# Kernel optimization log

Measured on AMD Instinct MI355X. Metric: run time of the kernel, lower is better.

## Reference

```python
import jax, jax.numpy as jnp
import numpy as np

N_NODES = 100000
N_EDGES = 800000
IN_FEATS = 128
NUM_CLASSES = 64


def setup_inputs() -> dict:
    key = jax.random.key(0)
    k1, k2, k3, k4 = jax.random.split(key, 4)
    x = jax.random.normal(k1, (N_NODES, IN_FEATS), dtype=jnp.float32)
    edge_src = jax.random.randint(k2, (N_EDGES,), 0, N_NODES, dtype=jnp.int64)
    edge_dst = jax.random.randint(k3, (N_EDGES,), 0, N_NODES, dtype=jnp.int64)
    W_neigh = jax.random.normal(k4, (NUM_CLASSES, IN_FEATS), dtype=jnp.float32) * (1.0 / np.sqrt(IN_FEATS))
    b_neigh = jnp.zeros((NUM_CLASSES,), dtype=jnp.float32)
    return {"x": x, "edge_src": edge_src, "edge_dst": edge_dst,
            "W_neigh": W_neigh, "b_neigh": b_neigh}


def reference(x, edge_src, edge_dst, W_neigh, b_neigh):
    # DGL SAGEConv with aggregator_type='gcn':
    #   h_neigh[v] = (sum_{u->v} x[u] + x[v]) / (in_degree(v) + 1)
    #   out = h_neigh @ W_neigh^T + b_neigh
    n = x.shape[0]
    # gather source features per edge, scatter-sum into destinations
    neigh_sum = jax.ops.segment_sum(x[edge_src], edge_dst, num_segments=n)  # [N, F]
    deg = jax.ops.segment_sum(jnp.ones((edge_src.shape[0],), dtype=x.dtype),
                              edge_dst, num_segments=n)                     # [N]
    h = (neigh_sum + x) / (deg + 1.0)[:, None]
    out = jnp.einsum('nf,cf->nc', h, W_neigh) + b_neigh
    return out
```

## Files before the change

### kernel.cpp

```cpp
#include <hip/hip_runtime.h>

#define N_NODES 100000
#define N_EDGES 800000
#define IN_FEATS 128
#define NUM_CLASSES 64

#define NSB    98
#define SCAP   9216
#define BINCAP 56
#define NBKT   12500
#define NBKT_PAD (NSB * 128)
#define HCAP   88
#define BKCAP  176

#define K1_GRID 1955

typedef short bf16x8 __attribute__((ext_vector_type(8)));
typedef float f32x4  __attribute__((ext_vector_type(4)));

static __device__ __forceinline__ unsigned short f2bf(float f) {
    unsigned u = __float_as_uint(f);
    unsigned r = (u + 0x7fffu + ((u >> 16) & 1u)) >> 16;
    return (unsigned short)r;
}
static __device__ __forceinline__ float bf2f(unsigned short v) {
    return __uint_as_float(((unsigned)v) << 16);
}

static __device__ __forceinline__ void gemm_body(char* smem, int gid,
                                                 const float* __restrict__ x,
                                                 const float* __restrict__ W,
                                                 unsigned short* __restrict__ y16) {
    const long base = (long)gid * 64;
    if (base >= N_NODES) return;

    unsigned short* Wf = (unsigned short*)smem;
    typedef unsigned short XsRow[136];
    XsRow* Xs = (XsRow*)(smem + 16384);

    const int tid = threadIdx.x;

    for (int i = tid; i < 4 * 4 * 64 * 8; i += 256) {
        const int j    = i & 7;
        const int lane = (i >> 3) & 63;
        const int t    = (i >> 9) & 3;
        const int s    = i >> 11;
        const int k = s * 32 + ((lane >> 4) << 3) + j;
        const int c = t * 16 + (lane & 15);
        Wf[i] = f2bf(W[c * IN_FEATS + k]);
    }

#pragma unroll
    for (int it = 0; it < 8; ++it) {
        const int i   = tid + it * 256;
        const int row = i >> 5;
        const int c4  = (i & 31) << 2;
        const long node = base + row;
        float4 v = make_float4(0.f, 0.f, 0.f, 0.f);
        if (node < N_NODES) v = *(const float4*)&x[node * IN_FEATS + c4];
        ushort4 w4;
        w4.x = f2bf(v.x); w4.y = f2bf(v.y); w4.z = f2bf(v.z); w4.w = f2bf(v.w);
        *(ushort4*)&Xs[row][c4] = w4;
    }
    __syncthreads();

    const int wave = tid >> 6;
    const int lane = tid & 63;
    const long nb  = base + wave * 16;

    bf16x8 wf[4][4];
#pragma unroll
    for (int s = 0; s < 4; ++s)
#pragma unroll
        for (int t = 0; t < 4; ++t)
            wf[s][t] = *(const bf16x8*)&Wf[(((s * 4 + t) * 64) + lane) * 8];

    f32x4 acc[4];
#pragma unroll
    for (int t = 0; t < 4; ++t) acc[t] = (f32x4){0.f, 0.f, 0.f, 0.f};

    const int m  = lane & 15;
    const int kq = lane >> 4;
    const unsigned short* arow = &Xs[wave * 16 + m][kq * 8];

#pragma unroll
    for (int s = 0; s < 4; ++s) {
        bf16x8 af = *(const bf16x8*)(arow + s * 32);
#pragma unroll
        for (int t = 0; t < 4; ++t)
            acc[t] = __builtin_amdgcn_mfma_f32_16x16x32_bf16(af, wf[s][t], acc[t], 0, 0, 0);
    }

    const int ccol  = lane & 15;
    const int rbase = (lane >> 4) << 2;
#pragma unroll
    for (int t = 0; t < 4; ++t) {
#pragma unroll
        for (int r = 0; r < 4; ++r) {
            const long n2 = nb + rbase + r;
            if (n2 < N_NODES)
                y16[n2 * NUM_CLASSES + t * 16 + ccol] = f2bf(acc[t][r]);
        }
    }
}

static __device__ __forceinline__ void p1_body(char* smem, int p1id,
                                               const int* __restrict__ esrc,
                                               const int* __restrict__ edst,
                                               int* __restrict__ sbcur,
                                               unsigned* __restrict__ stage) {
    typedef unsigned BinRow[BINCAP];
    BinRow* bins = (BinRow*)smem;
    int* bcnt  = (int*)(smem + 21952);
    int* bbase = (int*)(smem + 21952 + 392);

    const int tid = threadIdx.x;
    for (int i = tid; i < NSB; i += 256) bcnt[i] = 0;
    __syncthreads();

    const int e0 = p1id * 2048;
#pragma unroll
    for (int it = 0; it < 8; ++it) {
        const int e = e0 + it * 256 + tid;
        if (e < N_EDGES) {
            const unsigned s  = (unsigned)esrc[e];
            const unsigned d  = (unsigned)edst[e];
            const unsigned sb = d >> 10;
            const unsigned pk = s | ((d & 1023u) << 17);
            const int p = atomicAdd(&bcnt[sb], 1);
            if (p < BINCAP) {
                bins[sb][p] = pk;
            } else {
                const int gp = atomicAdd(&sbcur[sb << 4], 1);
                if (gp < SCAP) stage[sb * SCAP + gp] = pk;
            }
        }
    }
    __syncthreads();

    if (tid < NSB) {
        const int c = min(bcnt[tid], BINCAP);
        bcnt[tid]  = c;
        bbase[tid] = atomicAdd(&sbcur[tid << 4], c);
    }
    __syncthreads();

    for (int i = tid; i < NSB * BINCAP; i += 256) {
        const int sb = i / BINCAP;
        const int k  = i - sb * BINCAP;
        if (k < bcnt[sb]) {
            const int pos = bbase[sb] + k;
            if (pos < SCAP) stage[sb * SCAP + pos] = bins[sb][k];
        }
    }
}

__global__ __launch_bounds__(256) void k1_gemm_scatter(const float* __restrict__ x,
                                                       const float* __restrict__ W,
                                                       unsigned short* __restrict__ y16,
                                                       const int* __restrict__ esrc,
                                                       const int* __restrict__ edst,
                                                       int* __restrict__ sbcur,
                                                       unsigned* __restrict__ stage) {
    __shared__ __align__(16) char smem[33792];
    const int bid = blockIdx.x;
    const int r   = bid % 5;
    if (r == 4) {
        p1_body(smem, bid / 5, esrc, edst, sbcur, stage);
    } else {
        gemm_body(smem, (bid / 5) * 4 + r, x, W, y16);
    }
}

__global__ __launch_bounds__(256) void scatter_p2(const unsigned* __restrict__ stage,
                                                  const int* __restrict__ sbcur,
                                                  unsigned* __restrict__ pairs,
                                                  int* __restrict__ cnt_g) {
    __shared__ int lcnt[128];
    const int sb  = blockIdx.x >> 1;
    const int h   = blockIdx.x & 1;
    const int tid = threadIdx.x;

    if (tid < 128) lcnt[tid] = 0;
    __syncthreads();

    const int ecnt = min(sbcur[sb << 4], SCAP);
    const int half = (ecnt + 1) >> 1;
    const int lo   = h * half;
    const int hi   = min(ecnt, lo + half);

    const unsigned* sp = stage + (size_t)sb * SCAP;
    unsigned* pp = pairs + (size_t)sb * 128 * BKCAP + h * HCAP;

    for (int i = lo + tid; i < hi; i += 256) {
        const unsigned pk   = sp[i];
        const unsigned dlow = pk >> 17;
        const int fb = (int)(dlow >> 3);
        const unsigned dl = dlow & 7u;
        const int r = atomicAdd(&lcnt[fb], 1);
        if (r < HCAP) pp[fb * BKCAP + r] = (pk & 0x1FFFFu) | (dl << 20);
    }
    __syncthreads();

    if (tid < 128) cnt_g[((sb << 7) + tid) * 2 + h] = min(lcnt[tid], HCAP);
}

__global__ __launch_bounds__(256) void gather_bucket(const unsigned short* __restrict__ y16,
                                                     const unsigned* __restrict__ pairs,
                                                     const int* __restrict__ cnt_g,
                                                     const float* __restrict__ b,
                                                     float* __restrict__ out) {
    __shared__ float slab[4][8][64];
    __shared__ int   cnt[4][8];

    const int tid  = threadIdx.x;
    const int wave = tid >> 6;
    const int lane = tid & 63;
    const int bkt  = blockIdx.x;

    {
        float4* sz = (float4*)&slab[0][0][0];
        sz[tid]       = make_float4(0.f, 0.f, 0.f, 0.f);
        sz[tid + 256] = make_float4(0.f, 0.f, 0.f, 0.f);
    }

    const int half = wave >> 1;
    const int ws   = wave & 1;
    const int mh = cnt_g[bkt * 2 + half];
    const int q  = (mh + 1) >> 1;
    const int s0 = ws * q;
    const int s1 = min(mh, s0 + q);
    const int m  = max(0, s1 - s0);

    const unsigned* pb = pairs + (size_t)bkt * BKCAP + half * HCAP + s0;
    unsigned pr = 0;
    if (lane < m) pr = pb[lane];

    unsigned long long cnt64 = 0;
    __syncthreads();

    int j = 0;
    for (; j + 4 <= m; j += 4) {
        const unsigned p0 = __shfl(pr, j);
        const unsigned p1 = __shfl(pr, j + 1);
        const unsigned p2 = __shfl(pr, j + 2);
        const unsigned p3 = __shfl(pr, j + 3);
        const float v0 = bf2f(y16[(size_t)(p0 & 0xFFFFFu) * NUM_CLASSES + lane]);
        const float v1 = bf2f(y16[(size_t)(p1 & 0xFFFFFu) * NUM_CLASSES + lane]);
        const float v2 = bf2f(y16[(size_t)(p2 & 0xFFFFFu) * NUM_CLASSES + lane]);
        const float v3 = bf2f(y16[(size_t)(p3 & 0xFFFFFu) * NUM_CLASSES + lane]);
        slab[wave][p0 >> 20][lane] += v0;
        slab[wave][p1 >> 20][lane] += v1;
        slab[wave][p2 >> 20][lane] += v2;
        slab[wave][p3 >> 20][lane] += v3;
        cnt64 += (1ull << ((p0 >> 20) * 8)) + (1ull << ((p1 >> 20) * 8))
               + (1ull << ((p2 >> 20) * 8)) + (1ull << ((p3 >> 20) * 8));
    }
    for (; j < m; ++j) {
        const unsigned p = __shfl(pr, j);
        slab[wave][p >> 20][lane] += bf2f(y16[(size_t)(p & 0xFFFFFu) * NUM_CLASSES + lane]);
        cnt64 += 1ull << ((p >> 20) * 8);
    }

    if (lane < 8) cnt[wave][lane] = (int)((cnt64 >> (lane * 8)) & 0xFFull);
    __syncthreads();

    const int c = tid & 63;
#pragma unroll
    for (int i = 0; i < 2; ++i) {
        const int n = (tid >> 6) + 4 * i;
        const size_t v = ((size_t)bkt << 3) + n;
        const float s = slab[0][n][c] + slab[1][n][c] + slab[2][n][c] + slab[3][n][c];
        const int  dg = cnt[0][n] + cnt[1][n] + cnt[2][n] + cnt[3][n];
        const float self = bf2f(y16[v * NUM_CLASSES + c]);
        out[v * NUM_CLASSES + c] = (s + self) / (float)(dg + 1) + b[c];
    }
}

extern "C" void kernel_launch(void* const* d_in, const int* in_sizes, int n_in,
                              void* d_out, int out_size, void* d_ws, size_t ws_size,
                              hipStream_t stream) {
    const float* x    = (const float*)d_in[0];
    const int*   esrc = (const int*)d_in[1];
    const int*   edst = (const int*)d_in[2];
    const float* W    = (const float*)d_in[3];
    const float* b    = (const float*)d_in[4];
    float* out = (float*)d_out;

    char* p = (char*)d_ws;
    unsigned short* y16 = (unsigned short*)p;  p += (size_t)N_NODES * NUM_CLASSES * 2;
    unsigned* stage     = (unsigned*)p;        p += (size_t)NSB * SCAP * 4;
    unsigned* pairs     = (unsigned*)p;        p += (size_t)NBKT * BKCAP * 4;
    int* cnt_g          = (int*)p;             p += (size_t)NBKT_PAD * 2 * 4;
    int* sbcur          = (int*)p;             p += (size_t)NSB * 16 * 4;

    hipMemsetAsync(sbcur, 0, (size_t)NSB * 16 * 4, stream);

    k1_gemm_scatter<<<K1_GRID, 256, 0, stream>>>(x, W, y16, esrc, edst, sbcur, stage);

    scatter_p2<<<NSB * 2, 256, 0, stream>>>(stage, sbcur, pairs, cnt_g);

    gather_bucket<<<NBKT, 256, 0, stream>>>(y16, pairs, cnt_g, b, out);
}
```

Before: 158.2 us.

## Bin edges per destination node and gather with one wave per node

The second scatter pass now counts and stores source indices per individual destination node (1024 nodes per superblock, capped at 20 per half) instead of per 8-node bucket. The gather kernel assigns one wave per node, accumulating neighbour rows in registers and dropping the LDS slab, the per-bucket sync and the packed degree counters. This removes shared-memory read-modify-write traffic and barriers, at the cost of a larger LDS counter array and more scattered per-node writes in the scatter pass. The per-node cap of 40 could truncate very high in-degree nodes.

```diff
diff --git a/kernel.cpp b/kernel.cpp
--- a/kernel.cpp
+++ b/kernel.cpp
@@ -8,10 +8,8 @@
 #define NSB    98
 #define SCAP   9216
 #define BINCAP 56
-#define NBKT   12500
-#define NBKT_PAD (NSB * 128)
-#define HCAP   88
-#define BKCAP  176
+#define NCAP_H 20
+#define NODE_STRIDE 40
 
 #define K1_GRID 1955
 
@@ -176,12 +174,12 @@
                                                   const int* __restrict__ sbcur,
                                                   unsigned* __restrict__ pairs,
                                                   int* __restrict__ cnt_g) {
-    __shared__ int lcnt[128];
+    __shared__ int lcnt[1024];
     const int sb  = blockIdx.x >> 1;
     const int h   = blockIdx.x & 1;
     const int tid = threadIdx.x;
 
-    if (tid < 128) lcnt[tid] = 0;
+    for (int i = tid; i < 1024; i += 256) lcnt[i] = 0;
     __syncthreads();
 
     const int ecnt = min(sbcur[sb << 4], SCAP);
@@ -190,91 +188,58 @@
     const int hi   = min(ecnt, lo + half);
 
     const unsigned* sp = stage + (size_t)sb * SCAP;
-    unsigned* pp = pairs + (size_t)sb * 128 * BKCAP + h * HCAP;
 
     for (int i = lo + tid; i < hi; i += 256) {
-        const unsigned pk   = sp[i];
-        const unsigned dlow = pk >> 17;
-        const int fb = (int)(dlow >> 3);
-        const unsigned dl = dlow & 7u;
-        const int r = atomicAdd(&lcnt[fb], 1);
-        if (r < HCAP) pp[fb * BKCAP + r] = (pk & 0x1FFFFu) | (dl << 20);
-    }
-    __syncthreads();
-
-    if (tid < 128) cnt_g[((sb << 7) + tid) * 2 + h] = min(lcnt[tid], HCAP);
-}
-
-__global__ __launch_bounds__(256) void gather_bucket(const unsigned short* __restrict__ y16,
-                                                     const unsigned* __restrict__ pairs,
-                                                     const int* __restrict__ cnt_g,
-                                                     const float* __restrict__ b,
-                                                     float* __restrict__ out) {
-    __shared__ float slab[4][8][64];
-    __shared__ int   cnt[4][8];
-
-    const int tid  = threadIdx.x;
-    const int wave = tid >> 6;
-    const int lane = tid & 63;
-    const int bkt  = blockIdx.x;
-
-    {
-        float4* sz = (float4*)&slab[0][0][0];
-        sz[tid]       = make_float4(0.f, 0.f, 0.f, 0.f);
-        sz[tid + 256] = make_float4(0.f, 0.f, 0.f, 0.f);
-    }
-
-    const int half = wave >> 1;
-    const int ws   = wave & 1;
-    const int mh = cnt_g[bkt * 2 + half];
-    const int q  = (mh + 1) >> 1;
-    const int s0 = ws * q;
-    const int s1 = min(mh, s0 + q);
-    const int m  = max(0, s1 - s0);
-
-    const unsigned* pb = pairs + (size_t)bkt * BKCAP + half * HCAP + s0;
-    unsigned pr = 0;
-    if (lane < m) pr = pb[lane];
-
-    unsigned long long cnt64 = 0;
-    __syncthreads();
+        const unsigned pk = sp[i];
+        const int nl = (int)(pk >> 17);
+        const int r  = atomicAdd(&lcnt[nl], 1);
+        if (r < NCAP_H)
+            pairs[((size_t)(sb << 10) + nl) * NODE_STRIDE + h * NCAP_H + r] = pk & 0x1FFFFu;
+    }
+    __syncthreads();
+
+    for (int i = tid; i < 1024; i += 256)
+        cnt_g[(((sb << 10) + i) << 1) + h] = min(lcnt[i], NCAP_H);
+}
+
+__global__ __launch_bounds__(256) void gather_node(const unsigned short* __restrict__ y16,
+                                                   const unsigned* __restrict__ pairs,
+                                                   const int* __restrict__ cnt_g,
+                                                   const float* __restrict__ b,
+                                                   float* __restrict__ out) {
+    const int v = blockIdx.x * 4 + (threadIdx.x >> 6);
+    if (v >= N_NODES) return;
+    const int lane = threadIdx.x & 63;
+
+    const int da  = cnt_g[v * 2];
+    const int db  = cnt_g[v * 2 + 1];
+    const int deg = da + db;
+
+    const unsigned* base = pairs + (size_t)v * NODE_STRIDE;
+    unsigned idx = 0;
+    if (lane < deg)
+        idx = (lane < da) ? base[lane] : base[NCAP_H + (lane - da)];
+
+    float acc = bf2f(y16[(size_t)v * NUM_CLASSES + lane]);
 
     int j = 0;
-    for (; j + 4 <= m; j += 4) {
-        const unsigned p0 = __shfl(pr, j);
-        const unsigned p1 = __shfl(pr, j + 1);
-        const unsigned p2 = __shfl(pr, j + 2);
-        const unsigned p3 = __shfl(pr, j + 3);
-        const float v0 = bf2f(y16[(size_t)(p0 & 0xFFFFFu) * NUM_CLASSES + lane]);
-        const float v1 = bf2f(y16[(size_t)(p1 & 0xFFFFFu) * NUM_CLASSES + lane]);
-        const float v2 = bf2f(y16[(size_t)(p2 & 0xFFFFFu) * NUM_CLASSES + lane]);
-        const float v3 = bf2f(y16[(size_t)(p3 & 0xFFFFFu) * NUM_CLASSES + lane]);
-        slab[wave][p0 >> 20][lane] += v0;
-        slab[wave][p1 >> 20][lane] += v1;
-        slab[wave][p2 >> 20][lane] += v2;
-        slab[wave][p3 >> 20][lane] += v3;
-        cnt64 += (1ull << ((p0 >> 20) * 8)) + (1ull << ((p1 >> 20) * 8))
-               + (1ull << ((p2 >> 20) * 8)) + (1ull << ((p3 >> 20) * 8));
-    }
-    for (; j < m; ++j) {
-        const unsigned p = __shfl(pr, j);
-        slab[wave][p >> 20][lane] += bf2f(y16[(size_t)(p & 0xFFFFFu) * NUM_CLASSES + lane]);
-        cnt64 += 1ull << ((p >> 20) * 8);
-    }
-
-    if (lane < 8) cnt[wave][lane] = (int)((cnt64 >> (lane * 8)) & 0xFFull);
-    __syncthreads();
-
-    const int c = tid & 63;
-#pragma unroll
-    for (int i = 0; i < 2; ++i) {
-        const int n = (tid >> 6) + 4 * i;
-        const size_t v = ((size_t)bkt << 3) + n;
-        const float s = slab[0][n][c] + slab[1][n][c] + slab[2][n][c] + slab[3][n][c];
-        const int  dg = cnt[0][n] + cnt[1][n] + cnt[2][n] + cnt[3][n];
-        const float self = bf2f(y16[v * NUM_CLASSES + c]);
-        out[v * NUM_CLASSES + c] = (s + self) / (float)(dg + 1) + b[c];
-    }
+    for (; j + 4 <= deg; j += 4) {
+        const int s0 = __shfl((int)idx, j);
+        const int s1 = __shfl((int)idx, j + 1);
+        const int s2 = __shfl((int)idx, j + 2);
+        const int s3 = __shfl((int)idx, j + 3);
+        const float v0 = bf2f(y16[(size_t)s0 * NUM_CLASSES + lane]);
+        const float v1 = bf2f(y16[(size_t)s1 * NUM_CLASSES + lane]);
+        const float v2 = bf2f(y16[(size_t)s2 * NUM_CLASSES + lane]);
+        const float v3 = bf2f(y16[(size_t)s3 * NUM_CLASSES + lane]);
+        acc += (v0 + v1) + (v2 + v3);
+    }
+    for (; j < deg; ++j) {
+        const int s = __shfl((int)idx, j);
+        acc += bf2f(y16[(size_t)s * NUM_CLASSES + lane]);
+    }
+
+    out[(size_t)v * NUM_CLASSES + lane] = acc / (float)(deg + 1) + b[lane];
 }
 
 extern "C" void kernel_launch(void* const* d_in, const int* in_sizes, int n_in,
@@ -290,8 +255,8 @@
     char* p = (char*)d_ws;
     unsigned short* y16 = (unsigned short*)p;  p += (size_t)N_NODES * NUM_CLASSES * 2;
     unsigned* stage     = (unsigned*)p;        p += (size_t)NSB * SCAP * 4;
-    unsigned* pairs     = (unsigned*)p;        p += (size_t)NBKT * BKCAP * 4;
-    int* cnt_g          = (int*)p;             p += (size_t)NBKT_PAD * 2 * 4;
+    unsigned* pairs     = (unsigned*)p;        p += (size_t)NSB * 1024 * NODE_STRIDE * 4;
+    int* cnt_g          = (int*)p;             p += (size_t)NSB * 1024 * 2 * 4;
     int* sbcur          = (int*)p;             p += (size_t)NSB * 16 * 4;
 
     hipMemsetAsync(sbcur, 0, (size_t)NSB * 16 * 4, stream);
@@ -300,5 +265,5 @@
 
     scatter_p2<<<NSB * 2, 256, 0, stream>>>(stage, sbcur, pairs, cnt_g);
 
-    gather_bucket<<<NBKT, 256, 0, stream>>>(y16, pairs, cnt_g, b, out);
-}
+    gather_node<<<(N_NODES + 3) / 4, 256, 0, stream>>>(y16, pairs, cnt_g, b, out);
+}
```

After: 164.1 us. 3.7% more time.
